# Optimization experiments

Measured on AMD Instinct MI355X. Metric: run time of the kernel, lower is better.

Reference implementation:

```python
import jax, jax.numpy as jnp
import numpy as np

N, L, D = 4, 2048, 1024
H_DIM, OUT_DIM = 1024, 1024


def setup_inputs() -> dict:
    key = jax.random.key(0)
    ks = jax.random.split(key, 7)
    scale = 0.02
    return {
        "x": jax.random.normal(ks[0], (N, L, D), dtype=jnp.float32),
        "Wq": jax.random.normal(ks[1], (D, H_DIM), dtype=jnp.float32) * scale,
        "bq": jnp.zeros((H_DIM,), dtype=jnp.float32),
        "Wk": jax.random.normal(ks[2], (D, H_DIM), dtype=jnp.float32) * scale,
        "bk": jnp.zeros((H_DIM,), dtype=jnp.float32),
        "Wv": jax.random.normal(ks[3], (D, OUT_DIM), dtype=jnp.float32) * scale,
        "bv": jnp.zeros((OUT_DIM,), dtype=jnp.float32),
    }


def reference(x, Wq, bq, Wk, bk, Wv, bv):
    # q,k: [N,L,h_dim], v: [N,L,out_dim]
    q = jnp.einsum("nld,dh->nlh", x, Wq) + bq
    k = jnp.einsum("nld,dh->nlh", x, Wk) + bk
    v = jnp.einsum("nld,do->nlo", x, Wv) + bv
    # scores: [N,L,L]
    qk = jnp.einsum("nlh,nmh->nlm", q, k)
    # NOTE: original scales by sqrt(qk.shape[-1]) == sqrt(L) (seq len), not sqrt(h_dim)
    seq_len = qk.shape[-1]
    s = jax.nn.softmax(qk / jnp.sqrt(jnp.asarray(seq_len, dtype=qk.dtype)), axis=-1)
    return jnp.einsum("nlm,nmo->nlo", s, v)
```

## Files before the change

### kernel.cpp

```cpp
#include <hip/hip_runtime.h>
#include <hip/hip_bf16.h>


typedef __attribute__((ext_vector_type(8))) short bf16x8;
typedef __attribute__((ext_vector_type(4))) float f32x4;

#define AS_G(p) ((__attribute__((address_space(1))) void*)(p))
#define AS_L(p) ((__attribute__((address_space(3))) void*)(p))

__device__ __forceinline__ unsigned short f2bf(float f) {
  unsigned int u = __float_as_uint(f);
  unsigned int lsb = (u >> 16) & 1u;
  u += 0x7fffu + lsb;
  return (unsigned short)(u >> 16);
}

#define WAITV(n) asm volatile("s_waitcnt vmcnt(" #n ")" ::: "memory")
#define BARRIER() do { __builtin_amdgcn_s_barrier(); asm volatile("" ::: "memory"); } while (0)


#define S64A(ktk, rb, bofs)                                                   \
  __builtin_amdgcn_global_load_lds(                                           \
      AS_G(A + (size_t)(rowBase + (rb) * 64 + r0) * lda + (ktk) + goff),      \
      AS_L(lds + (bofs) + (rb) * 4096 + t * 8), 16, 0, 0)

#define S64B(ktk, rb, bofs)                                                   \
  __builtin_amdgcn_global_load_lds(                                           \
      AS_G(B + (size_t)(colBase + (rb) * 64 + r0) * ldb + (ktk) + goff),      \
      AS_L(lds + (bofs) + 16384 + (rb) * 4096 + t * 8), 16, 0, 0)

#define STAGE_TILE(ktk, bofs) do {                                            \
    S64A(ktk, 0, bofs); S64A(ktk, 1, bofs);                                   \
    S64A(ktk, 2, bofs); S64A(ktk, 3, bofs);                                   \
    S64B(ktk, 0, bofs); S64B(ktk, 1, bofs);                                   \
    S64B(ktk, 2, bofs); S64B(ktk, 3, bofs); } while (0)

#define LOAD_A(ih, bofs) do { _Pragma("unroll")                               \
    for (int ks_ = 0; ks_ < 2; ks_++) { _Pragma("unroll")                     \
      for (int ii = 0; ii < 4; ii++) {                                        \
        int row_ = wrow + ((ih) * 4 + ii) * 16 + r16;                         \
        int slot_ = (ks_ * 4 + q) ^ (r16 & 7);                                \
        af[ks_][ii] = *(const bf16x8*)(lds + (bofs) + row_ * 64 + slot_ * 8); \
      } } } while (0)

#define LOAD_B(jh, bofs) do { _Pragma("unroll")                               \
    for (int ks_ = 0; ks_ < 2; ks_++) { _Pragma("unroll")                     \
      for (int jj = 0; jj < 2; jj++) {                                        \
        int row_ = wcol + ((jh) * 2 + jj) * 16 + r16;                         \
        int slot_ = (ks_ * 4 + q) ^ (r16 & 7);                                \
        bfr[ks_][(jh) * 2 + jj] =                                             \
            *(const bf16x8*)(lds + (bofs) + 16384 + row_ * 64 + slot_ * 8);   \
      } } } while (0)

#define MM(ih, jh) do { __builtin_amdgcn_s_setprio(1); _Pragma("unroll")      \
    for (int ks_ = 0; ks_ < 2; ks_++) { _Pragma("unroll")                     \
      for (int ii = 0; ii < 4; ii++) { _Pragma("unroll")                      \
        for (int jj = 0; jj < 2; jj++)                                        \
          acc[(ih) * 4 + ii][(jh) * 2 + jj] =                                 \
              __builtin_amdgcn_mfma_f32_16x16x32_bf16(                        \
                  af[ks_][ii], bfr[ks_][(jh) * 2 + jj],                       \
                  acc[(ih) * 4 + ii][(jh) * 2 + jj], 0, 0, 0);                \
      } }                                                                     \
    __builtin_amdgcn_s_setprio(0); } while (0)

#define KTILE(ktc, bofs, ST) do {                                             \
                                                   \
    LOAD_A(0, bofs); LOAD_B(0, bofs);                                         \
    BARRIER(); MM(0, 0); BARRIER();                                           \
                            \
    LOAD_B(1, bofs);                                                          \
    if (ST) { S64A((ktc) + 128, 0, bofs); S64A((ktc) + 128, 2, bofs); }       \
    BARRIER(); MM(0, 1); BARRIER();                                           \
                            \
    LOAD_A(1, bofs);                                                          \
    if (ST) { S64B((ktc) + 128, 0, bofs); S64B((ktc) + 128, 1, bofs);         \
              S64B((ktc) + 128, 2, bofs); S64B((ktc) + 128, 3, bofs); }       \
    BARRIER(); MM(1, 1); BARRIER();                                           \
          \
    if (ST) { S64A((ktc) + 128, 1, bofs); S64A((ktc) + 128, 3, bofs); }       \
    BARRIER(); MM(1, 0);                                                      \
    if (ST) { WAITV(8); } else { WAITV(0); }                                  \
    BARRIER(); } while (0)

template <int EPI>
__global__ __launch_bounds__(512, 2) void gemm_8p(
    const unsigned short* __restrict__ A, const unsigned short* __restrict__ B,
    float* __restrict__ Cf, long long sA, long long sB, long long sC,
    int K, int lda, int ldb, int ldc,
    unsigned short* __restrict__ u0, unsigned short* __restrict__ u1,
    unsigned short* __restrict__ u2,
    const float* __restrict__ f0, const float* __restrict__ f1,
    const float* __restrict__ f2,
    float* __restrict__ rsum, float scale)
{
  __shared__ unsigned short lds[2 * 32768];

  const int t = threadIdx.x;
  const int rowBase = blockIdx.y * 256;
  const int colBase = blockIdx.x * 256;
  A += (long long)blockIdx.z * sA;
  B += (long long)blockIdx.z * sB;

  const int l = t & 63;
  const int w = t >> 6;
  const int wrow = (w >> 2) * 128;
  const int wcol = (w & 3) * 64;
  const int q = l >> 4;
  const int r16 = l & 15;

  const int r0 = t >> 3;
  const int goff = ((t & 7) ^ (r0 & 7)) << 3;

  f32x4 acc[8][4] = {};
  bf16x8 af[2][4], bfr[2][4];

  STAGE_TILE(0, 0);
  STAGE_TILE(64, 32768);
  WAITV(8);
  BARRIER();

  int kt = 0;
  for (; kt + 128 < K; kt += 128) {
    KTILE(kt, 0, 1);
    KTILE(kt + 64, 32768, 1);
  }
  KTILE(kt, 0, 0);
  KTILE(kt + 64, 32768, 0);

  if (EPI == 1) {
    unsigned short* p16 = u0 + (long long)blockIdx.z * sC;
    float* rs = rsum + (long long)blockIdx.z * 2048;
#pragma unroll
    for (int i = 0; i < 8; i++) {
#pragma unroll
      for (int r = 0; r < 4; r++) {
        int row = rowBase + wrow + i * 16 + q * 4 + r;
        float rowpart = 0.f;
#pragma unroll
        for (int j = 0; j < 4; j++) {
          int col = colBase + wcol + j * 16 + r16;
          float e = __expf(acc[i][j][r] * scale);
          p16[(size_t)row * ldc + col] = f2bf(e);
          rowpart += e;
        }
#pragma unroll
        for (int m = 1; m < 16; m <<= 1) rowpart += __shfl_xor(rowpart, m);
        if (r16 == 0) atomicAdd(rs + row, rowpart);
      }
    }
  } else if (EPI == 2) {
    const int seg = colBase >> 10;
    if (seg < 2) {
      unsigned short* dst = seg ? u1 : u0;
      const float* bias = seg ? f1 : f0;
      const int cb = colBase & 1023;
#pragma unroll
      for (int i = 0; i < 8; i++) {
#pragma unroll
        for (int r = 0; r < 4; r++) {
          int row = rowBase + wrow + i * 16 + q * 4 + r;
#pragma unroll
          for (int j = 0; j < 4; j++) {
            int col = cb + wcol + j * 16 + r16;
            dst[(size_t)row * 1024 + col] = f2bf(acc[i][j][r] + bias[col]);
          }
        }
      }
    } else {
      const int ob = colBase - 2048;
#pragma unroll
      for (int i = 0; i < 8; i++) {
        int posBase = rowBase + wrow + i * 16 + q * 4;
        int b = posBase >> 11;
        int pos = posBase & 2047;
#pragma unroll
        for (int j = 0; j < 4; j++) {
          int o = ob + wcol + j * 16 + r16;
          float bias = f2[o];
          ushort4 pk;
          pk.x = f2bf(acc[i][j][0] + bias);
          pk.y = f2bf(acc[i][j][1] + bias);
          pk.z = f2bf(acc[i][j][2] + bias);
          pk.w = f2bf(acc[i][j][3] + bias);
          *(ushort4*)(u2 + ((size_t)((b << 10) + o) * 2048 + pos)) = pk;
        }
      }
    }
  } else {
    float* C = Cf + (long long)blockIdx.z * sC;
    const float* rs = rsum + (long long)blockIdx.z * 2048;
#pragma unroll
    for (int i = 0; i < 8; i++) {
#pragma unroll
      for (int r = 0; r < 4; r++) {
        int row = rowBase + wrow + i * 16 + q * 4 + r;
        float inv = 1.0f / rs[row];
#pragma unroll
        for (int j = 0; j < 4; j++) {
          int col = colBase + wcol + j * 16 + r16;
          C[(size_t)row * ldc + col] = acc[i][j][r] * inv;
        }
      }
    }
  }
}


__global__ __launch_bounds__(256) void cast_f32_to_bf16(
    const float* __restrict__ in, unsigned short* __restrict__ out, int n4,
    float* __restrict__ rzero, int nz4)
{
  int i = blockIdx.x * 256 + threadIdx.x;
  if (i < nz4) ((float4*)rzero)[i] = make_float4(0.f, 0.f, 0.f, 0.f);
  if (i >= n4) return;
  float4 v = ((const float4*)in)[i];
  ushort4 o;
  o.x = f2bf(v.x); o.y = f2bf(v.y); o.z = f2bf(v.z); o.w = f2bf(v.w);
  ((ushort4*)out)[i] = o;
}


__global__ __launch_bounds__(256) void wtrans(
    const float* __restrict__ Wq, const float* __restrict__ Wk,
    const float* __restrict__ Wv, unsigned short* __restrict__ WT)
{
  __shared__ float tile[32][33];
  const float* in = blockIdx.z == 0 ? Wq : (blockIdx.z == 1 ? Wk : Wv);
  unsigned short* out = WT + (size_t)blockIdx.z * 1024 * 1024;
  const int bc = blockIdx.x * 32;
  const int br = blockIdx.y * 32;
  const int tx = threadIdx.x;
  const int ty = threadIdx.y;
#pragma unroll
  for (int i = 0; i < 4; i++)
    tile[ty + i * 8][tx] = in[(size_t)(br + ty + i * 8) * 1024 + bc + tx];
  __syncthreads();
#pragma unroll
  for (int i = 0; i < 4; i++)
    out[(size_t)(bc + ty + i * 8) * 1024 + br + tx] = f2bf(tile[tx][ty + i * 8]);
}


extern "C" void kernel_launch(void* const* d_in, const int* in_sizes, int n_in,
                              void* d_out, int out_size, void* d_ws, size_t ws_size,
                              hipStream_t stream) {
  (void)in_sizes; (void)n_in; (void)out_size;

  const float* x  = (const float*)d_in[0];
  const float* Wq = (const float*)d_in[1];
  const float* bq = (const float*)d_in[2];
  const float* Wk = (const float*)d_in[3];
  const float* bk = (const float*)d_in[4];
  const float* Wv = (const float*)d_in[5];
  const float* bv = (const float*)d_in[6];
  float* out = (float*)d_out;

  const int Nb = 4, L = 2048, D = 1024, H = 1024, O = 1024;
  const int M = Nb * L;
  const int NQKV = 3 * H;

  char* ws = (char*)d_ws;
  size_t off = 0;
  unsigned short* xb = (unsigned short*)(ws + off); off += (size_t)M * D * 2;
  unsigned short* qb = (unsigned short*)(ws + off); off += (size_t)M * H * 2;
  unsigned short* kb = (unsigned short*)(ws + off); off += (size_t)M * H * 2;
  unsigned short* vt = (unsigned short*)(ws + off); off += (size_t)M * O * 2;
  unsigned short* WT = (unsigned short*)(ws + off); off += (size_t)NQKV * D * 2;
  unsigned short* P  = (unsigned short*)(ws + off); off += (size_t)Nb * L * L * 2;
  float* rsum = (float*)(ws + off); off += (size_t)Nb * L * 4;
  if (ws_size < off) return;

  dim3 blk256(256);
  dim3 blk512(512);

  cast_f32_to_bf16<<<(M * D / 4 + 255) / 256, blk256, 0, stream>>>(
      x, xb, M * D / 4, rsum, Nb * L / 4);

  wtrans<<<dim3(32, 32, 3), dim3(32, 8), 0, stream>>>(Wq, Wk, Wv, WT);

  gemm_8p<2><<<dim3(NQKV / 256, M / 256, 1), blk512, 0, stream>>>(
      xb, WT, nullptr, 0, 0, 0, D, D, D, 0,
      qb, kb, vt, bq, bk, bv, nullptr, 0.f);

  gemm_8p<1><<<dim3(L / 256, L / 256, Nb), blk512, 0, stream>>>(
      qb, kb, nullptr, (long long)L * H, (long long)L * H, (long long)L * L,
      H, H, H, L,
      P, nullptr, nullptr, nullptr, nullptr, nullptr,
      rsum, 0.022097086912079608f );

  gemm_8p<3><<<dim3(O / 256, L / 256, Nb), blk512, 0, stream>>>(
      P, vt, out, (long long)L * L, (long long)O * L, (long long)L * O,
      L, L, L, O,
      nullptr, nullptr, nullptr, nullptr, nullptr, nullptr,
      rsum, 0.f);
}
```

Before: 256.4 us.

## Restructure GEMM k-loop into two-phase pipeline with fewer barriers

Replaces the four-phase k-tile schedule (eight barriers per tile) with a two-phase schedule holding one barrier per half-tile. It issues the next-tile global-to-LDS loads across the two halves, including a deferred A-row pair into the other buffer, and adds sched_barrier fences around s_barrier. The aim is to cut barrier stalls and overlap more MFMA work with loads, at the cost of tighter LDS hazard reasoning and a changed waitcnt count (6 instead of 8).

```diff
diff --git a/kernel.cpp b/kernel.cpp
--- a/kernel.cpp
+++ b/kernel.cpp
@@ -16,7 +16,10 @@
 }
 
 #define WAITV(n) asm volatile("s_waitcnt vmcnt(" #n ")" ::: "memory")
-#define BARRIER() do { __builtin_amdgcn_s_barrier(); asm volatile("" ::: "memory"); } while (0)
+#define BARRIER() do { asm volatile("" ::: "memory");                         \
+    __builtin_amdgcn_s_barrier();                                             \
+    asm volatile("" ::: "memory");                                            \
+    __builtin_amdgcn_sched_barrier(0); } while (0)
 
 
 #define S64A(ktk, rb, bofs)                                                   \
@@ -63,27 +66,27 @@
       } }                                                                     \
     __builtin_amdgcn_s_setprio(0); } while (0)
 
-#define KTILE(ktc, bofs, ST) do {                                             \
-                                                   \
-    LOAD_A(0, bofs); LOAD_B(0, bofs);                                         \
-    BARRIER(); MM(0, 0); BARRIER();                                           \
-                            \
-    LOAD_B(1, bofs);                                                          \
-    if (ST) { S64A((ktc) + 128, 0, bofs); S64A((ktc) + 128, 2, bofs); }       \
-    BARRIER(); MM(0, 1); BARRIER();                                           \
-                            \
+#define TILE(ktc, bofs, obofs) do {                                           \
+                                                                      \
+    LOAD_A(0, bofs); LOAD_B(0, bofs); LOAD_B(1, bofs);                        \
+    if ((ktc) && (ktc) + 64 < K) {                                            \
+      S64A((ktc) + 64, 1, obofs); S64A((ktc) + 64, 3, obofs);                 \
+    }                                                                         \
+    MM(0, 0); MM(0, 1);                                                       \
+    BARRIER();                                                                \
+                                                                      \
     LOAD_A(1, bofs);                                                          \
-    if (ST) { S64B((ktc) + 128, 0, bofs); S64B((ktc) + 128, 1, bofs);         \
-              S64B((ktc) + 128, 2, bofs); S64B((ktc) + 128, 3, bofs); }       \
-    BARRIER(); MM(1, 1); BARRIER();                                           \
-          \
-    if (ST) { S64A((ktc) + 128, 1, bofs); S64A((ktc) + 128, 3, bofs); }       \
-    BARRIER(); MM(1, 0);                                                      \
-    if (ST) { WAITV(8); } else { WAITV(0); }                                  \
+    if ((ktc) + 128 < K) {                                                    \
+      S64A((ktc) + 128, 0, bofs); S64A((ktc) + 128, 2, bofs);                 \
+      S64B((ktc) + 128, 0, bofs); S64B((ktc) + 128, 1, bofs);                 \
+      S64B((ktc) + 128, 2, bofs); S64B((ktc) + 128, 3, bofs);                 \
+    }                                                                         \
+    MM(1, 1); MM(1, 0);                                                       \
+    if ((ktc) + 128 < K) { WAITV(6); } else { WAITV(0); }                     \
     BARRIER(); } while (0)
 
 template <int EPI>
-__global__ __launch_bounds__(512, 2) void gemm_8p(
+__global__ __launch_bounds__(512, 2) void gemm_2r(
     const unsigned short* __restrict__ A, const unsigned short* __restrict__ B,
     float* __restrict__ Cf, long long sA, long long sB, long long sC,
     int K, int lda, int ldb, int ldc,
@@ -119,13 +122,10 @@
   WAITV(8);
   BARRIER();
 
-  int kt = 0;
-  for (; kt + 128 < K; kt += 128) {
-    KTILE(kt, 0, 1);
-    KTILE(kt + 64, 32768, 1);
+  for (int kt = 0; kt < K; kt += 128) {
+    TILE(kt, 0, 32768);
+    TILE(kt + 64, 32768, 0);
   }
-  KTILE(kt, 0, 0);
-  KTILE(kt + 64, 32768, 0);
 
   if (EPI == 1) {
     unsigned short* p16 = u0 + (long long)blockIdx.z * sC;
@@ -278,17 +278,17 @@
 
   wtrans<<<dim3(32, 32, 3), dim3(32, 8), 0, stream>>>(Wq, Wk, Wv, WT);
 
-  gemm_8p<2><<<dim3(NQKV / 256, M / 256, 1), blk512, 0, stream>>>(
+  gemm_2r<2><<<dim3(NQKV / 256, M / 256, 1), blk512, 0, stream>>>(
       xb, WT, nullptr, 0, 0, 0, D, D, D, 0,
       qb, kb, vt, bq, bk, bv, nullptr, 0.f);
 
-  gemm_8p<1><<<dim3(L / 256, L / 256, Nb), blk512, 0, stream>>>(
+  gemm_2r<1><<<dim3(L / 256, L / 256, Nb), blk512, 0, stream>>>(
       qb, kb, nullptr, (long long)L * H, (long long)L * H, (long long)L * L,
       H, H, H, L,
       P, nullptr, nullptr, nullptr, nullptr, nullptr,
       rsum, 0.022097086912079608f );
 
-  gemm_8p<3><<<dim3(O / 256, L / 256, Nb), blk512, 0, stream>>>(
+  gemm_2r<3><<<dim3(O / 256, L / 256, Nb), blk512, 0, stream>>>(
       P, vt, out, (long long)L * L, (long long)O * L, (long long)L * O,
       L, L, L, O,
       nullptr, nullptr, nullptr, nullptr, nullptr, nullptr,
```

Result: no change. 253.0 us (-1.3%).
